# Optimization experiments

Measured on AMD Instinct MI355X. Metric: run time of the kernel, lower is better.

The kernel has to match this reference:

```python
import jax, jax.numpy as jnp
import numpy as np

N_EMBED = 512
E_DIM = 256
BETA = 0.25


def setup_inputs() -> dict:
    key = jax.random.key(0)
    k1, k2 = jax.random.split(key)
    z = jax.random.normal(k1, (32, 16, 16, 16, E_DIM), dtype=jnp.float32)
    embedding = jax.random.normal(k2, (N_EMBED, E_DIM), dtype=jnp.float32)
    return {"z": z, "embedding": embedding}


def reference(z, embedding):
    # Flatten spatial/batch dims: [N, e_dim]
    zf = z.reshape(-1, E_DIM)
    # similarity = ||z||^2 + ||e||^2 - 2 z.e  (squared distances)
    sim = (
        jnp.sum(zf * zf, axis=1, keepdims=True)
        + jnp.sum(embedding * embedding, axis=1)
        - 2.0 * jnp.einsum("bd,nd->bn", zf, embedding)
    )
    # NOTE: original code uses argmax (farthest code) -- faithfully reproduced.
    codebook_idxs = jnp.argmax(sim, axis=-1)
    # histogram side-effect: codebook_hist[idx] += 1
    hist = jnp.zeros((N_EMBED,), dtype=jnp.float32).at[codebook_idxs].add(1.0)
    z_q = embedding[codebook_idxs].reshape(z.shape)
    vq_loss = jnp.mean((z_q - jax.lax.stop_gradient(z)) ** 2)
    commitment_loss = BETA * jnp.mean((jax.lax.stop_gradient(z_q) - z) ** 2)
    # straight-through estimator
    z_q_st = z + jax.lax.stop_gradient(z_q - z)
    return (z_q_st, vq_loss, commitment_loss, codebook_idxs, hist)
```

## Files before the change

### kernel.cpp

```cpp
#include <hip/hip_runtime.h>
#include <hip/hip_bf16.h>

#define D 256
#define NC 512
#define NROWS 131072L

#define OFF_ZQ   0L
#define OFF_VQ   33554432L
#define OFF_CM   33554433L
#define OFF_IDX  33554434L
#define OFF_HIST 33685506L

#define WS_LPART 0
#define WS_HIST  2048
#define WS_E2    2560
#define WS_CNT   3072
#define WS_AMB   3136
#define WS_FIDX  134208
#define WS_BK    265280
#define WS_NEED  (330816L * 4)

#define MARGIN 1.25f

typedef __attribute__((ext_vector_type(8))) short bf16x8;
typedef __attribute__((ext_vector_type(4))) float f32x4;

#define AS1 __attribute__((address_space(1)))
#define AS3 __attribute__((address_space(3)))

__device__ __forceinline__ unsigned short f2bf(float f) {
    union { float f; unsigned int u; } a; a.f = f;
    return (unsigned short)((a.u + 0x7FFFu + ((a.u >> 16) & 1u)) >> 16);
}

__global__ void vq_init(float* __restrict__ ws) {
    int i = blockIdx.x * 1024 + threadIdx.x;
    if (i < 3073) ws[i] = 0.0f;
}

__global__ void vq_e2(const float* __restrict__ e, float* __restrict__ e2) {
    int c = blockIdx.x;
    int l = threadIdx.x;
    float4 v = *(const float4*)(e + c * D + l * 4);
    float s = v.x * v.x + v.y * v.y + v.z * v.z + v.w * v.w;
    #pragma unroll
    for (int off = 32; off; off >>= 1) s += __shfl_xor(s, off);
    if (l == 0) e2[c] = s;
}

__global__ void vq_convB(const float* __restrict__ e, unsigned short* __restrict__ Bk,
                         float* __restrict__ e2) {
    __shared__ float r4[4];
    int code = blockIdx.x, k = threadIdx.x;
    float v = e[code * D + k];
    Bk[((k >> 5) * NC + code) * 32 + (k & 31)] = f2bf(v);
    float s = v * v;
    #pragma unroll
    for (int off = 32; off; off >>= 1) s += __shfl_xor(s, off);
    if ((k & 63) == 0) r4[k >> 6] = s;
    __syncthreads();
    if (k == 0) e2[code] = r4[0] + r4[1] + r4[2] + r4[3];
}

__global__ __launch_bounds__(512, 4)
void vq_gemm(const float* __restrict__ z, const unsigned short* __restrict__ Bk,
             const float* __restrict__ e2, int* __restrict__ fidx,
             int* __restrict__ acnt, int* __restrict__ alist) {
    __shared__ __align__(16) unsigned short zh[64 * 264];
    __shared__ float red[64 * 25];

    const int tid = threadIdx.x;
    const int w = tid >> 6, l = tid & 63, q = l >> 4, ln = l & 15;
    const long row0 = (long)blockIdx.x * 64;

    #pragma unroll
    for (int j = 0; j < 8; ++j) {
        int c = j * 512 + tid;
        int row = c >> 6, c4 = (c & 63) * 4;
        float4 av = *(const float4*)(z + (row0 + row) * D + c4);
        *(ushort4*)&zh[row * 264 + c4] =
            make_ushort4(f2bf(av.x), f2bf(av.y), f2bf(av.z), f2bf(av.w));
    }
    __syncthreads();

    const unsigned short* bbase = Bk + ((w * 64 + ln) * 32 + q * 8);
    const unsigned short* abase = &zh[ln * 264 + q * 8];

    f32x4 acc[4][4];
    #pragma unroll
    for (int mt = 0; mt < 4; ++mt)
        #pragma unroll
        for (int nt = 0; nt < 4; ++nt) acc[mt][nt] = (f32x4){0.f, 0.f, 0.f, 0.f};

    #pragma unroll
    for (int s = 0; s < 8; ++s) {
        const unsigned short* bs = bbase + s * (NC * 32);
        bf16x8 bfr[4], af[4];
        #pragma unroll
        for (int nt = 0; nt < 4; ++nt)
            bfr[nt] = *(const bf16x8*)(bs + nt * (16 * 32));
        #pragma unroll
        for (int mt = 0; mt < 4; ++mt)
            af[mt] = *(const bf16x8*)(abase + mt * (16 * 264) + s * 32);
        #pragma unroll
        for (int mt = 0; mt < 4; ++mt)
            #pragma unroll
            for (int nt = 0; nt < 4; ++nt)
                acc[mt][nt] = __builtin_amdgcn_mfma_f32_16x16x32_bf16(af[mt], bfr[nt], acc[mt][nt], 0, 0, 0);
    }

    float e2v[4];
    #pragma unroll
    for (int nt = 0; nt < 4; ++nt) e2v[nt] = e2[w * 64 + nt * 16 + ln];

    #pragma unroll
    for (int mt = 0; mt < 4; ++mt) {
        #pragma unroll
        for (int r = 0; r < 4; ++r) {
            float v1 = -3.0e38f, v2 = -3.0e38f; int i1 = 0;
            #pragma unroll
            for (int nt = 0; nt < 4; ++nt) {
                float v = e2v[nt] - 2.0f * acc[mt][nt][r];
                int c = w * 64 + nt * 16 + ln;
                if (v > v1) { v2 = v1; v1 = v; i1 = c; }
                else if (v > v2) v2 = v;
            }
            #pragma unroll
            for (int off = 1; off < 16; off <<= 1) {
                float ov1 = __shfl_xor(v1, off);
                float ov2 = __shfl_xor(v2, off);
                int   oi1 = __shfl_xor(i1, off);
                if (ov1 > v1 || (ov1 == v1 && oi1 < i1)) {
                    v2 = fmaxf(v1, ov2); v1 = ov1; i1 = oi1;
                } else {
                    v2 = fmaxf(v2, ov1);
                }
            }
            if (ln == 0) {
                int rr = mt * 16 + q * 4 + r;
                red[rr * 25 + w * 3 + 0] = v1;
                red[rr * 25 + w * 3 + 1] = (float)i1;
                red[rr * 25 + w * 3 + 2] = v2;
            }
        }
    }
    __syncthreads();
    if (tid < 64) {
        float v1 = -3.0e38f, v2 = -3.0e38f; int i1 = 0;
        #pragma unroll
        for (int g = 0; g < 8; ++g) {
            float rv1 = red[tid * 25 + g * 3 + 0];
            int   ri  = (int)red[tid * 25 + g * 3 + 1];
            float rv2 = red[tid * 25 + g * 3 + 2];
            if (rv1 > v1) { v2 = fmaxf(v1, rv2); v1 = rv1; i1 = ri; }
            else v2 = fmaxf(v2, rv1);
        }
        fidx[row0 + tid] = i1;
        if (v1 - v2 < MARGIN) {
            int ppos = atomicAdd(acnt, 1);
            alist[ppos] = (int)(row0 + tid);
        }
    }
}

__global__ __launch_bounds__(256, 2)
void vq_refine(const float* __restrict__ z, const float* __restrict__ e,
               const float* __restrict__ e2, const int* __restrict__ acnt,
               const int* __restrict__ alist, int* __restrict__ fidx) {
    __shared__ __align__(16) float z_s[32][D];
    __shared__ __align__(16) float e_s[16][NC + 4];
    __shared__ int rowg[32];
    __shared__ int idx_s[32];
    const int tid = threadIdx.x, lane = tid & 63, w = tid >> 6;
    const int cnt = *acnt;
    for (int g = blockIdx.x; g * 32 < cnt; g += gridDim.x) {
        const int base = g * 32;
        __syncthreads();
        if (tid < 32) rowg[tid] = alist[min(base + tid, cnt - 1)];
        __syncthreads();
        #pragma unroll
        for (int j = 0; j < 8; ++j) {
            int c = j * 256 + tid, rl = c >> 6, c4 = (c & 63) * 4;
            *(float4*)&z_s[rl][c4] = *(const float4*)(z + (long)rowg[rl] * D + c4);
        }
        float acc[8][8];
        #pragma unroll
        for (int r = 0; r < 8; ++r)
            #pragma unroll
            for (int c = 0; c < 8; ++c) acc[r][c] = 0.0f;
        const int r0 = w * 8, c_lo = lane * 4;
        for (int kc = 0; kc < D; kc += 16) {
            __syncthreads();
            #pragma unroll
            for (int p = 0; p < 8; ++p) {
                int c = p * 64 + (tid >> 2), kk4 = (tid & 3) * 4;
                float4 v = *(const float4*)(e + c * D + kc + kk4);
                e_s[kk4 + 0][c] = v.x; e_s[kk4 + 1][c] = v.y;
                e_s[kk4 + 2][c] = v.z; e_s[kk4 + 3][c] = v.w;
            }
            __syncthreads();
            #pragma unroll
            for (int k4 = 0; k4 < 16; k4 += 4) {
                float zr[8][4];
                #pragma unroll
                for (int r = 0; r < 8; ++r) *(float4*)zr[r] = *(const float4*)&z_s[r0 + r][kc + k4];
                #pragma unroll
                for (int kk = 0; kk < 4; ++kk) {
                    float ev[8];
                    *(float4*)&ev[0] = *(const float4*)&e_s[k4 + kk][c_lo];
                    *(float4*)&ev[4] = *(const float4*)&e_s[k4 + kk][c_lo + 256];
                    #pragma unroll
                    for (int r = 0; r < 8; ++r)
                        #pragma unroll
                        for (int c = 0; c < 8; ++c) acc[r][c] = fmaf(zr[r][kk], ev[c], acc[r][c]);
                }
            }
        }
        float e2v[8];
        #pragma unroll
        for (int gg = 0; gg < 2; ++gg)
            #pragma unroll
            for (int i = 0; i < 4; ++i) e2v[gg * 4 + i] = e2[gg * 256 + c_lo + i];
        #pragma unroll
        for (int r = 0; r < 8; ++r) {
            float bvv = -3.0e38f; int bc = 0;
            #pragma unroll
            for (int c = 0; c < 8; ++c) {
                int col = (c >> 2) * 256 + c_lo + (c & 3);
                float v = e2v[c] - 2.0f * acc[r][c];
                if (v > bvv) { bvv = v; bc = col; }
            }
            #pragma unroll
            for (int off = 32; off; off >>= 1) {
                float ov = __shfl_xor(bvv, off); int oc = __shfl_xor(bc, off);
                if (ov > bvv || (ov == bvv && oc < bc)) { bvv = ov; bc = oc; }
            }
            if (lane == 0) idx_s[r0 + r] = bc;
        }
        __syncthreads();
        if (tid < 32 && base + tid < cnt) fidx[rowg[tid]] = idx_s[tid];
    }
}

__global__ __launch_bounds__(256)
void vq_hist(const int* __restrict__ fidx, float* __restrict__ out,
             float* __restrict__ hist) {
    __shared__ int h[NC];
    const int t = threadIdx.x;
    h[t] = 0; h[t + 256] = 0;
    __syncthreads();
    const long base = (long)blockIdx.x * 2048;
    #pragma unroll
    for (int j = 0; j < 8; ++j) {
        long i = base + j * 256 + t;
        int idx = fidx[i];
        out[OFF_IDX + i] = (float)idx;
        atomicAdd(&h[idx], 1);
    }
    __syncthreads();
    #pragma unroll
    for (int j = 0; j < 2; ++j) {
        int k = j * 256 + t;
        int c = h[k];
        if (c) atomicAdd(&hist[k], (float)c);
    }
}

__global__ __launch_bounds__(256)
void vq_epi(const float* __restrict__ z, const float* __restrict__ e,
            const int* __restrict__ fidx, float* __restrict__ out,
            float* __restrict__ lpart) {
    __shared__ int idxs[64];
    __shared__ float rs[4];
    const int t = threadIdx.x, lane = t & 63, w = t >> 6;
    const long row0 = (long)blockIdx.x * 64;
    if (t < 64) idxs[t] = fidx[row0 + t];
    __syncthreads();
    float ls = 0.f;
    #pragma unroll 4
    for (int j = 0; j < 16; ++j) {
        const int r = w * 16 + j;
        const long row = row0 + r;
        const int idx = idxs[r];
        float4 zv = *(const float4*)(z + row * D + lane * 4);
        float4 ev = *(const float4*)(e + (long)idx * D + lane * 4);
        float4 dq;
        dq.x = ev.x - zv.x; dq.y = ev.y - zv.y; dq.z = ev.z - zv.z; dq.w = ev.w - zv.w;
        float4 o;
        o.x = zv.x + dq.x; o.y = zv.y + dq.y; o.z = zv.z + dq.z; o.w = zv.w + dq.w;
        *(float4*)(out + OFF_ZQ + row * D + lane * 4) = o;
        ls += dq.x * dq.x + dq.y * dq.y + dq.z * dq.z + dq.w * dq.w;
    }
    #pragma unroll
    for (int off = 32; off; off >>= 1) ls += __shfl_xor(ls, off);
    if (lane == 0) rs[w] = ls;
    __syncthreads();
    if (t == 0) lpart[blockIdx.x] = rs[0] + rs[1] + rs[2] + rs[3];
}

__global__ void vq_fin(const float* __restrict__ ws, float* __restrict__ out) {
    __shared__ float sred[16];
    const int t = threadIdx.x, lane = t & 63, w = t >> 6;
    float s = ws[WS_LPART + t] + ws[WS_LPART + t + 1024];
    #pragma unroll
    for (int off = 32; off; off >>= 1) s += __shfl_xor(s, off);
    if (lane == 0) sred[w] = s;
    __syncthreads();
    if (t == 0) {
        float tot = 0.f;
        #pragma unroll
        for (int i = 0; i < 16; ++i) tot += sred[i];
        float m = tot / 33554432.0f;
        out[OFF_VQ] = m;
        out[OFF_CM] = 0.25f * m;
    }
    if (t < NC) out[OFF_HIST + t] = ws[WS_HIST + t];
}

__global__ __launch_bounds__(256, 2)
void vq_main_fb(const float* __restrict__ z, const float* __restrict__ e,
                const float* __restrict__ e2, float* __restrict__ out,
                float* __restrict__ ws_loss, float* __restrict__ ws_hist) {
    __shared__ __align__(16) float z_s[32][D];
    __shared__ __align__(16) float e_s[16][NC + 4];
    __shared__ int   idx_s[32];
    __shared__ float red_s[4];
    const int tid = threadIdx.x, lane = tid & 63, w = tid >> 6;
    const long row0 = (long)blockIdx.x * 32;
    {
        const float4* zg = (const float4*)(z + row0 * D);
        float4* zs = (float4*)(&z_s[0][0]);
        #pragma unroll
        for (int i = 0; i < 8; ++i) zs[i * 256 + tid] = zg[i * 256 + tid];
    }
    float acc[8][8];
    #pragma unroll
    for (int r = 0; r < 8; ++r)
        #pragma unroll
        for (int c = 0; c < 8; ++c) acc[r][c] = 0.0f;
    const int r0 = w * 8, c_lo = lane * 4;
    for (int kc = 0; kc < D; kc += 16) {
        __syncthreads();
        #pragma unroll
        for (int p = 0; p < 8; ++p) {
            int c = p * 64 + (tid >> 2), kk4 = (tid & 3) * 4;
            float4 v = *(const float4*)(e + c * D + kc + kk4);
            e_s[kk4 + 0][c] = v.x; e_s[kk4 + 1][c] = v.y;
            e_s[kk4 + 2][c] = v.z; e_s[kk4 + 3][c] = v.w;
        }
        __syncthreads();
        #pragma unroll
        for (int k4 = 0; k4 < 16; k4 += 4) {
            float zr[8][4];
            #pragma unroll
            for (int r = 0; r < 8; ++r) *(float4*)zr[r] = *(const float4*)&z_s[r0 + r][kc + k4];
            #pragma unroll
            for (int kk = 0; kk < 4; ++kk) {
                float ev[8];
                *(float4*)&ev[0] = *(const float4*)&e_s[k4 + kk][c_lo];
                *(float4*)&ev[4] = *(const float4*)&e_s[k4 + kk][c_lo + 256];
                #pragma unroll
                for (int r = 0; r < 8; ++r)
                    #pragma unroll
                    for (int c = 0; c < 8; ++c) acc[r][c] = fmaf(zr[r][kk], ev[c], acc[r][c]);
            }
        }
    }
    float e2v[8];
    #pragma unroll
    for (int g = 0; g < 2; ++g)
        #pragma unroll
        for (int i = 0; i < 4; ++i) e2v[g * 4 + i] = e2[g * 256 + c_lo + i];
    #pragma unroll
    for (int r = 0; r < 8; ++r) {
        float bvv = -3.0e38f; int bc = 0;
        #pragma unroll
        for (int c = 0; c < 8; ++c) {
            int col = (c >> 2) * 256 + c_lo + (c & 3);
            float v = e2v[c] - 2.0f * acc[r][c];
            if (v > bvv) { bvv = v; bc = col; }
        }
        #pragma unroll
        for (int off = 32; off; off >>= 1) {
            float ov = __shfl_xor(bvv, off); int oc = __shfl_xor(bc, off);
            if (ov > bvv || (ov == bvv && oc < bc)) { bvv = ov; bc = oc; }
        }
        if (lane == 0) idx_s[r0 + r] = bc;
    }
    __syncthreads();
    if (tid < 32) {
        int bc = idx_s[tid];
        out[OFF_IDX + row0 + tid] = (float)bc;
        atomicAdd(&ws_hist[bc], 1.0f);
    }
    float lsum = 0.0f;
    for (int r = 0; r < 32; ++r) {
        int idx = idx_s[r];
        float ev = e[idx * D + tid];
        float zv = z_s[r][tid];
        float dq = ev - zv;
        out[OFF_ZQ + (row0 + r) * D + tid] = zv + dq;
        lsum += dq * dq;
    }
    #pragma unroll
    for (int off = 32; off; off >>= 1) lsum += __shfl_xor(lsum, off);
    if (lane == 0) red_s[w] = lsum;
    __syncthreads();
    if (tid == 0) atomicAdd(ws_loss, red_s[0] + red_s[1] + red_s[2] + red_s[3]);
}

__global__ void vq_init_fb(float* __restrict__ ws) {
    int t = threadIdx.x;
    if (t < 513) ws[t] = 0.0f;
}
__global__ void vq_fin_fb(const float* __restrict__ ws, float* __restrict__ out) {
    int t = blockIdx.x * blockDim.x + threadIdx.x;
    if (t < NC) out[OFF_HIST + t] = ws[1 + t];
    if (t == NC) {
        float m = ws[0] / 33554432.0f;
        out[OFF_VQ] = m; out[OFF_CM] = 0.25f * m;
    }
}

extern "C" void kernel_launch(void* const* d_in, const int* in_sizes, int n_in,
                              void* d_out, int out_size, void* d_ws, size_t ws_size,
                              hipStream_t stream) {
    const float* z = (const float*)d_in[0];
    const float* e = (const float*)d_in[1];
    float* out = (float*)d_out;
    float* ws  = (float*)d_ws;

    if (ws_size >= (size_t)WS_NEED) {
        float* lpart = ws + WS_LPART;
        float* hist  = ws + WS_HIST;
        float* e2    = ws + WS_E2;
        int*   acnt  = (int*)(ws + WS_CNT);
        int*   alist = (int*)(ws + WS_AMB);
        int*   fidx  = (int*)(ws + WS_FIDX);
        unsigned short* Bk = (unsigned short*)(ws + WS_BK);

        vq_init<<<4, 1024, 0, stream>>>(ws);
        vq_convB<<<NC, 256, 0, stream>>>(e, Bk, e2);
        vq_gemm<<<2048, 512, 0, stream>>>(z, Bk, e2, fidx, acnt, alist);
        vq_refine<<<512, 256, 0, stream>>>(z, e, e2, acnt, alist, fidx);
        vq_hist<<<64, 256, 0, stream>>>(fidx, out, hist);
        vq_epi<<<2048, 256, 0, stream>>>(z, e, fidx, out, lpart);
        vq_fin<<<1, 1024, 0, stream>>>(ws, out);
    } else {
        float* ws_loss = ws;
        float* ws_hist = ws + 1;
        float* ws_e2   = ws + 513;
        vq_init_fb<<<1, 1024, 0, stream>>>(ws);
        vq_e2<<<NC, 64, 0, stream>>>(e, ws_e2);
        vq_main_fb<<<4096, 256, 0, stream>>>(z, e, ws_e2, out, ws_loss, ws_hist);
        vq_fin_fb<<<3, 256, 0, stream>>>(ws, out);
    }
}
```

Before: 402.5 us.

## Fuse histogram and quantized-output epilogue into GEMM, patch ambiguous rows in refine

```diff
diff --git a/kernel.cpp b/kernel.cpp
--- a/kernel.cpp
+++ b/kernel.cpp
@@ -15,6 +15,7 @@
 #define WS_HIST  2048
 #define WS_E2    2560
 #define WS_CNT   3072
+#define WS_LCORR 3073
 #define WS_AMB   3136
 #define WS_FIDX  134208
 #define WS_BK    265280
@@ -35,7 +36,7 @@
 
 __global__ void vq_init(float* __restrict__ ws) {
     int i = blockIdx.x * 1024 + threadIdx.x;
-    if (i < 3073) ws[i] = 0.0f;
+    if (i < 3074) ws[i] = 0.0f;
 }
 
 __global__ void vq_e2(const float* __restrict__ e, float* __restrict__ e2) {
@@ -64,10 +65,14 @@
 
 __global__ __launch_bounds__(512, 4)
 void vq_gemm(const float* __restrict__ z, const unsigned short* __restrict__ Bk,
-             const float* __restrict__ e2, int* __restrict__ fidx,
-             int* __restrict__ acnt, int* __restrict__ alist) {
+             const float* __restrict__ e2, const float* __restrict__ e,
+             int* __restrict__ fidx, int* __restrict__ acnt, int* __restrict__ alist,
+             float* __restrict__ hist, float* __restrict__ lpart,
+             float* __restrict__ out) {
     __shared__ __align__(16) unsigned short zh[64 * 264];
     __shared__ float red[64 * 25];
+    __shared__ int idx_s[64];
+    __shared__ float rs[8];
 
     const int tid = threadIdx.x;
     const int w = tid >> 6, l = tid & 63, q = l >> 4, ln = l & 15;
@@ -155,22 +160,58 @@
             if (rv1 > v1) { v2 = fmaxf(v1, rv2); v1 = rv1; i1 = ri; }
             else v2 = fmaxf(v2, rv1);
         }
+        int amb = (v1 - v2 < MARGIN) ? 1 : 0;
+        idx_s[tid] = i1 | (amb << 16);
         fidx[row0 + tid] = i1;
-        if (v1 - v2 < MARGIN) {
+        out[OFF_IDX + row0 + tid] = (float)i1;
+        atomicAdd(&hist[i1], 1.0f);
+        if (amb) {
             int ppos = atomicAdd(acnt, 1);
             alist[ppos] = (int)(row0 + tid);
         }
+    }
+    __syncthreads();
+
+    float ls = 0.f;
+    #pragma unroll
+    for (int j = 0; j < 8; ++j) {
+        const int r = w * 8 + j;
+        const long row = row0 + r;
+        const int v = idx_s[r];
+        const int idx = v & 0xFFFF;
+        float4 zv = *(const float4*)(z + row * D + l * 4);
+        float4 ev = *(const float4*)(e + (long)idx * D + l * 4);
+        float4 dq;
+        dq.x = ev.x - zv.x; dq.y = ev.y - zv.y; dq.z = ev.z - zv.z; dq.w = ev.w - zv.w;
+        float4 o;
+        o.x = zv.x + dq.x; o.y = zv.y + dq.y; o.z = zv.z + dq.z; o.w = zv.w + dq.w;
+        *(float4*)(out + OFF_ZQ + row * D + l * 4) = o;
+        if (!(v >> 16))
+            ls += dq.x * dq.x + dq.y * dq.y + dq.z * dq.z + dq.w * dq.w;
+    }
+    #pragma unroll
+    for (int off = 32; off; off >>= 1) ls += __shfl_xor(ls, off);
+    if (l == 0) rs[w] = ls;
+    __syncthreads();
+    if (tid == 0) {
+        float t = 0.f;
+        #pragma unroll
+        for (int i = 0; i < 8; ++i) t += rs[i];
+        lpart[blockIdx.x] = t;
     }
 }
 
 __global__ __launch_bounds__(256, 2)
 void vq_refine(const float* __restrict__ z, const float* __restrict__ e,
                const float* __restrict__ e2, const int* __restrict__ acnt,
-               const int* __restrict__ alist, int* __restrict__ fidx) {
+               const int* __restrict__ alist, const int* __restrict__ fidx,
+               float* __restrict__ hist, float* __restrict__ lcorr,
+               float* __restrict__ out) {
     __shared__ __align__(16) float z_s[32][D];
     __shared__ __align__(16) float e_s[16][NC + 4];
     __shared__ int rowg[32];
     __shared__ int idx_s[32];
+    __shared__ float rs2[4];
     const int tid = threadIdx.x, lane = tid & 63, w = tid >> 6;
     const int cnt = *acnt;
     for (int g = blockIdx.x; g * 32 < cnt; g += gridDim.x) {
@@ -238,64 +279,37 @@
             if (lane == 0) idx_s[r0 + r] = bc;
         }
         __syncthreads();
-        if (tid < 32 && base + tid < cnt) fidx[rowg[tid]] = idx_s[tid];
-    }
-}
-
-__global__ __launch_bounds__(256)
-void vq_hist(const int* __restrict__ fidx, float* __restrict__ out,
-             float* __restrict__ hist) {
-    __shared__ int h[NC];
-    const int t = threadIdx.x;
-    h[t] = 0; h[t + 256] = 0;
-    __syncthreads();
-    const long base = (long)blockIdx.x * 2048;
-    #pragma unroll
-    for (int j = 0; j < 8; ++j) {
-        long i = base + j * 256 + t;
-        int idx = fidx[i];
-        out[OFF_IDX + i] = (float)idx;
-        atomicAdd(&h[idx], 1);
-    }
-    __syncthreads();
-    #pragma unroll
-    for (int j = 0; j < 2; ++j) {
-        int k = j * 256 + t;
-        int c = h[k];
-        if (c) atomicAdd(&hist[k], (float)c);
-    }
-}
-
-__global__ __launch_bounds__(256)
-void vq_epi(const float* __restrict__ z, const float* __restrict__ e,
-            const int* __restrict__ fidx, float* __restrict__ out,
-            float* __restrict__ lpart) {
-    __shared__ int idxs[64];
-    __shared__ float rs[4];
-    const int t = threadIdx.x, lane = t & 63, w = t >> 6;
-    const long row0 = (long)blockIdx.x * 64;
-    if (t < 64) idxs[t] = fidx[row0 + t];
-    __syncthreads();
-    float ls = 0.f;
-    #pragma unroll 4
-    for (int j = 0; j < 16; ++j) {
-        const int r = w * 16 + j;
-        const long row = row0 + r;
-        const int idx = idxs[r];
-        float4 zv = *(const float4*)(z + row * D + lane * 4);
-        float4 ev = *(const float4*)(e + (long)idx * D + lane * 4);
-        float4 dq;
-        dq.x = ev.x - zv.x; dq.y = ev.y - zv.y; dq.z = ev.z - zv.z; dq.w = ev.w - zv.w;
-        float4 o;
-        o.x = zv.x + dq.x; o.y = zv.y + dq.y; o.z = zv.z + dq.z; o.w = zv.w + dq.w;
-        *(float4*)(out + OFF_ZQ + row * D + lane * 4) = o;
-        ls += dq.x * dq.x + dq.y * dq.y + dq.z * dq.z + dq.w * dq.w;
-    }
-    #pragma unroll
-    for (int off = 32; off; off >>= 1) ls += __shfl_xor(ls, off);
-    if (lane == 0) rs[w] = ls;
-    __syncthreads();
-    if (t == 0) lpart[blockIdx.x] = rs[0] + rs[1] + rs[2] + rs[3];
+        float ls = 0.f;
+        #pragma unroll
+        for (int j = 0; j < 8; ++j) {
+            const int r = w * 8 + j;
+            const bool valid = (base + r < cnt);
+            const int row = rowg[r];
+            const int nb = idx_s[r];
+            float4 zv = *(const float4*)&z_s[r][lane * 4];
+            float4 ev = *(const float4*)(e + (long)nb * D + lane * 4);
+            float4 dq;
+            dq.x = ev.x - zv.x; dq.y = ev.y - zv.y; dq.z = ev.z - zv.z; dq.w = ev.w - zv.w;
+            if (valid)
+                ls += dq.x * dq.x + dq.y * dq.y + dq.z * dq.z + dq.w * dq.w;
+            const int ob = fidx[row];
+            if (valid && nb != ob) {
+                float4 o;
+                o.x = zv.x + dq.x; o.y = zv.y + dq.y; o.z = zv.z + dq.z; o.w = zv.w + dq.w;
+                *(float4*)(out + OFF_ZQ + (long)row * D + lane * 4) = o;
+                if (lane == 0) {
+                    out[OFF_IDX + row] = (float)nb;
+                    atomicAdd(&hist[ob], -1.0f);
+                    atomicAdd(&hist[nb], 1.0f);
+                }
+            }
+        }
+        #pragma unroll
+        for (int off = 32; off; off >>= 1) ls += __shfl_xor(ls, off);
+        if (lane == 0) rs2[w] = ls;
+        __syncthreads();
+        if (tid == 0) atomicAdd(lcorr, rs2[0] + rs2[1] + rs2[2] + rs2[3]);
+    }
 }
 
 __global__ void vq_fin(const float* __restrict__ ws, float* __restrict__ out) {
@@ -307,7 +321,7 @@
     if (lane == 0) sred[w] = s;
     __syncthreads();
     if (t == 0) {
-        float tot = 0.f;
+        float tot = ws[WS_LCORR];
         #pragma unroll
         for (int i = 0; i < 16; ++i) tot += sred[i];
         float m = tot / 33554432.0f;
@@ -385,7 +399,7 @@
             float ov = __shfl_xor(bvv, off); int oc = __shfl_xor(bc, off);
             if (ov > bvv || (ov == bvv && oc < bc)) { bvv = ov; bc = oc; }
         }
-        if (lane == 0) idx_s[r0 + r] = bc;
+        if (lane == 0) idx_s[r] = bc;
     }
     __syncthreads();
     if (tid < 32) {
@@ -435,16 +449,15 @@
         float* hist  = ws + WS_HIST;
         float* e2    = ws + WS_E2;
         int*   acnt  = (int*)(ws + WS_CNT);
+        float* lcorr = ws + WS_LCORR;
         int*   alist = (int*)(ws + WS_AMB);
         int*   fidx  = (int*)(ws + WS_FIDX);
         unsigned short* Bk = (unsigned short*)(ws + WS_BK);
 
         vq_init<<<4, 1024, 0, stream>>>(ws);
         vq_convB<<<NC, 256, 0, stream>>>(e, Bk, e2);
-        vq_gemm<<<2048, 512, 0, stream>>>(z, Bk, e2, fidx, acnt, alist);
-        vq_refine<<<512, 256, 0, stream>>>(z, e, e2, acnt, alist, fidx);
-        vq_hist<<<64, 256, 0, stream>>>(fidx, out, hist);
-        vq_epi<<<2048, 256, 0, stream>>>(z, e, fidx, out, lpart);
+        vq_gemm<<<2048, 512, 0, stream>>>(z, Bk, e2, e, fidx, acnt, alist, hist, lpart, out);
+        vq_refine<<<512, 256, 0, stream>>>(z, e, e2, acnt, alist, fidx, hist, lcorr, out);
         vq_fin<<<1, 1024, 0, stream>>>(ws, out);
     } else {
         float* ws_loss = ws;
```

Result: slower. 555.2 us (+37.9%).
